# Kernel optimization log

Hardware: AMD Instinct MI355X
Metric: run time of the kernel (lower is better)

The kernel has to match this reference:

```python
import jax, jax.numpy as jnp
import numpy as np

H = 1.0  # RBF bandwidth (init kwarg h)


def setup_inputs() -> dict:
    key = jax.random.key(0)
    k1, k2 = jax.random.split(key)
    x = jax.random.normal(k1, (8192, 512), dtype=jnp.float32)
    x1 = jax.random.normal(k2, (8192, 512), dtype=jnp.float32)
    return {"x": x, "x1": x1}


def reference(x, x1):
    # exp(-||x_i - x1_j||^2 / h), computed via the GEMM trick to avoid the
    # O(N*M*D) broadcast intermediate the original torch code materializes.
    x_sq = jnp.sum(x * x, axis=-1, keepdims=True)          # [N, 1]
    x1_sq = jnp.sum(x1 * x1, axis=-1)                       # [M]
    cross = jnp.einsum('nd,md->nm', x, x1)                  # [N, M]
    d = jnp.maximum(x_sq + x1_sq[None, :] - 2.0 * cross, 0.0)
    return jnp.exp(-d / H)
```

## Files before the change

kernel.cpp:

```cpp
#include <hip/hip_runtime.h>
#include <stdint.h>
#include <stddef.h>


#define NROWS 8192
#define DIMK  512
#define BM    128
#define BN    128
#define BKB   128
#define KT    (DIMK / BKB)

typedef __bf16 bf16x8 __attribute__((ext_vector_type(8)));
typedef int    i32x8  __attribute__((ext_vector_type(8)));
typedef float  f32x4  __attribute__((ext_vector_type(4)));

#define AS1 __attribute__((address_space(1)))
#define AS3 __attribute__((address_space(3)))

__device__ __forceinline__ uint32_t f2bf(float f) {
    uint32_t u = __float_as_uint(f);
    return (u + 0x7FFFu + ((u >> 16) & 1u)) >> 16;
}

__device__ __forceinline__ uint32_t f2e4m3(float f) {
    uint32_t u   = __float_as_uint(f);
    uint32_t s   = (u >> 24) & 0x80u;
    uint32_t abs = u & 0x7FFFFFFFu;
    if (abs >= 0x43E00000u)
        return s | 0x7Eu;
    if (abs < 0x3C800000u) {
        uint32_t m = (uint32_t)rintf(__uint_as_float(abs) * 512.0f);
        return s | m;
    }
    uint32_t lsb = (abs >> 20) & 1u;
    uint32_t r   = abs + 0x7FFFFu + lsb;
    uint32_t e   = (r >> 23) - 127u + 7u;
    uint32_t m   = (r >> 20) & 7u;
    return s | (e << 3) | m;
}

__global__ __launch_bounds__(256) void precast_fp8(
    const float* __restrict__ x, const float* __restrict__ x1,
    uint8_t* __restrict__ xf, uint8_t* __restrict__ x1f,
    float* __restrict__ xsq, float* __restrict__ x1sq)
{
    const int w    = threadIdx.x >> 6;
    const int lane = threadIdx.x & 63;
    const int row  = blockIdx.x * 4 + w;
    const float* src;
    uint8_t* dstb;
    float* dsts;
    if (blockIdx.y == 0) { src = x  + (size_t)row * DIMK; dstb = xf  + (size_t)row * DIMK; dsts = xsq  + row; }
    else                 { src = x1 + (size_t)row * DIMK; dstb = x1f + (size_t)row * DIMK; dsts = x1sq + row; }

    float4 v0 = ((const float4*)src)[lane * 2];
    float4 v1 = ((const float4*)src)[lane * 2 + 1];
    float s = v0.x * v0.x + v0.y * v0.y + v0.z * v0.z + v0.w * v0.w
            + v1.x * v1.x + v1.y * v1.y + v1.z * v1.z + v1.w * v1.w;

    uint2 p;
    p.x = f2e4m3(v0.x) | (f2e4m3(v0.y) << 8) | (f2e4m3(v0.z) << 16) | (f2e4m3(v0.w) << 24);
    p.y = f2e4m3(v1.x) | (f2e4m3(v1.y) << 8) | (f2e4m3(v1.z) << 16) | (f2e4m3(v1.w) << 24);
    ((uint2*)dstb)[lane] = p;

    #pragma unroll
    for (int off = 32; off > 0; off >>= 1) s += __shfl_down(s, off);
    if (lane == 0) *dsts = s;
}

__global__ __launch_bounds__(256) void norms_only(
    const float* __restrict__ x, const float* __restrict__ x1,
    float* __restrict__ xsq, float* __restrict__ x1sq)
{
    const int row = blockIdx.x;
    const float* src = (blockIdx.y == 0) ? x + (size_t)row * DIMK : x1 + (size_t)row * DIMK;
    float* dsts      = (blockIdx.y == 0) ? xsq + row : x1sq + row;
    const int t = threadIdx.x;
    float2 v = ((const float2*)src)[t];
    float s = v.x * v.x + v.y * v.y;
    #pragma unroll
    for (int off = 32; off > 0; off >>= 1) s += __shfl_down(s, off);
    __shared__ float red[4];
    if ((t & 63) == 0) red[t >> 6] = s;
    __syncthreads();
    if (t == 0) *dsts = red[0] + red[1] + red[2] + red[3];
}

__global__ __launch_bounds__(256) void rbf_mfma_mxfp8(
    const uint8_t* __restrict__ Xf, const uint8_t* __restrict__ X1f,
    const float* __restrict__ xsq, const float* __restrict__ x1sq,
    float* __restrict__ out)
{
    __shared__ uint8_t As[BM * BKB];
    __shared__ uint8_t Bs[BN * BKB];

    const int t    = threadIdx.x;
    const int bm   = blockIdx.x;
    const int bn   = blockIdx.y;
    const int lane = t & 63;
    const int w    = t >> 6;
    const int wm   = w >> 1;
    const int wn   = w & 1;

    const int srow = t >> 3;
    const int scol = (t & 7) * 16;
    const uint8_t* gA = Xf  + (size_t)(bm * BM + srow) * DIMK + scol;
    const uint8_t* gB = X1f + (size_t)(bn * BN + srow) * DIMK + scol;
    uint8_t* lA = &As[t * 16];
    uint8_t* lB = &Bs[t * 16];

    const int lrow = lane & 15;
    const int row0 = bm * BM + wm * 64 + (lane >> 4) * 4;
    const int col0 = bn * BN + wn * 64 + lrow;
    float xs[4][4], x1s[4];
    #pragma unroll
    for (int tm = 0; tm < 4; ++tm)
        #pragma unroll
        for (int r = 0; r < 4; ++r) xs[tm][r] = xsq[row0 + tm * 16 + r];
    #pragma unroll
    for (int tn = 0; tn < 4; ++tn) x1s[tn] = x1sq[col0 + tn * 16];

    f32x4 acc[4][4];
    #pragma unroll
    for (int i = 0; i < 4; ++i)
        #pragma unroll
        for (int j = 0; j < 4; ++j)
            acc[i][j] = f32x4{0.f, 0.f, 0.f, 0.f};

    const int kq = (lane >> 4) * 32;
    int aoff[4], boff[4];
    #pragma unroll
    for (int i = 0; i < 4; ++i) {
        aoff[i] = (wm * 64 + i * 16 + lrow) * BKB + kq;
        boff[i] = (wn * 64 + i * 16 + lrow) * BKB + kq;
    }

    #pragma unroll
    for (int kt = 0; kt < KT; ++kt) {
        const uint8_t* ga = gA + kt * BKB;
        const uint8_t* gb = gB + kt * BKB;
        #pragma unroll
        for (int c = 0; c < 4; ++c) {
            __builtin_amdgcn_global_load_lds((AS1 void*)(ga + (size_t)c * 32 * DIMK),
                                             (AS3 void*)(lA + c * 4096), 16, 0, 0);
            __builtin_amdgcn_global_load_lds((AS1 void*)(gb + (size_t)c * 32 * DIMK),
                                             (AS3 void*)(lB + c * 4096), 16, 0, 0);
        }
        __syncthreads();

        i32x8 af[4], bg[4];
        #pragma unroll
        for (int i = 0; i < 4; ++i) af[i] = *(const i32x8*)&As[aoff[i]];
        #pragma unroll
        for (int i = 0; i < 4; ++i) bg[i] = *(const i32x8*)&Bs[boff[i]];
        #pragma unroll
        for (int i = 0; i < 4; ++i)
            #pragma unroll
            for (int j = 0; j < 4; ++j)
                acc[i][j] = __builtin_amdgcn_mfma_scale_f32_16x16x128_f8f6f4(
                    af[i], bg[j], acc[i][j],
                    0, 0,
                    0, 0x7F7F7F7F,
                    0, 0x7F7F7F7F);
        __syncthreads();
    }

    #pragma unroll
    for (int tm = 0; tm < 4; ++tm)
        #pragma unroll
        for (int tn = 0; tn < 4; ++tn)
            #pragma unroll
            for (int r = 0; r < 4; ++r) {
                const int row = row0 + tm * 16 + r;
                const int col = col0 + tn * 16;
                float d = xs[tm][r] + x1s[tn] - 2.0f * acc[tm][tn][r];
                d = fmaxf(d, 0.0f);
                out[(size_t)row * NROWS + col] = __expf(-d);
            }
}

__global__ __launch_bounds__(256) void rbf_mfma_inline(
    const float* __restrict__ X, const float* __restrict__ X1,
    const float* __restrict__ xsq, const float* __restrict__ x1sq,
    float* __restrict__ out)
{
    __shared__ uint16_t As[BM * 32];
    __shared__ uint16_t Bs[BN * 32];

    const int t    = threadIdx.x;
    const int bm   = blockIdx.x;
    const int bn   = blockIdx.y;
    const int lane = t & 63;
    const int w    = t >> 6;
    const int wm   = w >> 1;
    const int wn   = w & 1;

    f32x4 acc[4][4];
    #pragma unroll
    for (int i = 0; i < 4; ++i)
        #pragma unroll
        for (int j = 0; j < 4; ++j)
            acc[i][j] = f32x4{0.f, 0.f, 0.f, 0.f};

    const int lrow = lane & 15;
    const int kq   = (lane >> 4) * 8;
    int aoff[4], boff[4];
    #pragma unroll
    for (int i = 0; i < 4; ++i) {
        aoff[i] = (wm * 64 + i * 16 + lrow) * 32 + kq;
        boff[i] = (wn * 64 + i * 16 + lrow) * 32 + kq;
    }

    for (int kt = 0; kt < DIMK / 32; ++kt) {
        #pragma unroll
        for (int i = 0; i < 4; ++i) {
            const int g   = t + i * 256;
            const int row = g >> 3;
            const int c4  = (g & 7) * 4;
            float4 va = *(const float4*)&X [(size_t)(bm * BM + row) * DIMK + kt * 32 + c4];
            float4 vb = *(const float4*)&X1[(size_t)(bn * BN + row) * DIMK + kt * 32 + c4];
            uint2 pa, pb;
            pa.x = f2bf(va.x) | (f2bf(va.y) << 16);
            pa.y = f2bf(va.z) | (f2bf(va.w) << 16);
            pb.x = f2bf(vb.x) | (f2bf(vb.y) << 16);
            pb.y = f2bf(vb.z) | (f2bf(vb.w) << 16);
            *(uint2*)&As[g * 4] = pa;
            *(uint2*)&Bs[g * 4] = pb;
        }
        __syncthreads();

        bf16x8 af[4], bg[4];
        #pragma unroll
        for (int i = 0; i < 4; ++i) af[i] = *(const bf16x8*)&As[aoff[i]];
        #pragma unroll
        for (int i = 0; i < 4; ++i) bg[i] = *(const bf16x8*)&Bs[boff[i]];
        #pragma unroll
        for (int i = 0; i < 4; ++i)
            #pragma unroll
            for (int j = 0; j < 4; ++j)
                acc[i][j] = __builtin_amdgcn_mfma_f32_16x16x32_bf16(af[i], bg[j], acc[i][j], 0, 0, 0);
        __syncthreads();
    }

    const int row0 = bm * BM + wm * 64 + (lane >> 4) * 4;
    const int col0 = bn * BN + wn * 64 + lrow;
    float xs[4][4], x1s[4];
    #pragma unroll
    for (int tm = 0; tm < 4; ++tm)
        #pragma unroll
        for (int r = 0; r < 4; ++r) xs[tm][r] = xsq[row0 + tm * 16 + r];
    #pragma unroll
    for (int tn = 0; tn < 4; ++tn) x1s[tn] = x1sq[col0 + tn * 16];

    #pragma unroll
    for (int tm = 0; tm < 4; ++tm)
        #pragma unroll
        for (int tn = 0; tn < 4; ++tn)
            #pragma unroll
            for (int r = 0; r < 4; ++r) {
                const int row = row0 + tm * 16 + r;
                const int col = col0 + tn * 16;
                float d = xs[tm][r] + x1s[tn] - 2.0f * acc[tm][tn][r];
                d = fmaxf(d, 0.0f);
                out[(size_t)row * NROWS + col] = __expf(-d);
            }
}

extern "C" void kernel_launch(void* const* d_in, const int* in_sizes, int n_in,
                              void* d_out, int out_size, void* d_ws, size_t ws_size,
                              hipStream_t stream)
{
    const float* x  = (const float*)d_in[0];
    const float* x1 = (const float*)d_in[1];
    float* out = (float*)d_out;

    const size_t f8_bytes  = (size_t)NROWS * DIMK;
    const size_t need_full = 2 * f8_bytes + 2 * (size_t)NROWS * sizeof(float);

    dim3 gridG(NROWS / BM, NROWS / BN);

    if (ws_size >= need_full) {
        uint8_t* xf   = (uint8_t*)d_ws;
        uint8_t* x1f  = xf + f8_bytes;
        float*   xsq  = (float*)((char*)d_ws + 2 * f8_bytes);
        float*   x1sq = xsq + NROWS;
        precast_fp8<<<dim3(NROWS / 4, 2), 256, 0, stream>>>(x, x1, xf, x1f, xsq, x1sq);
        rbf_mfma_mxfp8<<<gridG, 256, 0, stream>>>(xf, x1f, xsq, x1sq, out);
    } else {
        float* xsq  = (float*)d_ws;
        float* x1sq = xsq + NROWS;
        norms_only<<<dim3(NROWS, 2), 256, 0, stream>>>(x, x1, xsq, x1sq);
        rbf_mfma_inline<<<gridG, 256, 0, stream>>>(x, x1, xsq, x1sq, out);
    }
}
```

Measured before the change: 314.2 us.

## Use hardware fp8 conversion, tune occupancy, defer norm loads, nontemporal output stores

```diff
diff --git a/kernel.cpp b/kernel.cpp
--- a/kernel.cpp
+++ b/kernel.cpp
@@ -22,21 +22,10 @@
     return (u + 0x7FFFu + ((u >> 16) & 1u)) >> 16;
 }
 
-__device__ __forceinline__ uint32_t f2e4m3(float f) {
-    uint32_t u   = __float_as_uint(f);
-    uint32_t s   = (u >> 24) & 0x80u;
-    uint32_t abs = u & 0x7FFFFFFFu;
-    if (abs >= 0x43E00000u)
-        return s | 0x7Eu;
-    if (abs < 0x3C800000u) {
-        uint32_t m = (uint32_t)rintf(__uint_as_float(abs) * 512.0f);
-        return s | m;
-    }
-    uint32_t lsb = (abs >> 20) & 1u;
-    uint32_t r   = abs + 0x7FFFFu + lsb;
-    uint32_t e   = (r >> 23) - 127u + 7u;
-    uint32_t m   = (r >> 20) & 7u;
-    return s | (e << 3) | m;
+__device__ __forceinline__ uint32_t pk_fp8x4(float a, float b, float c, float d) {
+    int w = __builtin_amdgcn_cvt_pk_fp8_f32(a, b, 0, false);
+    w     = __builtin_amdgcn_cvt_pk_fp8_f32(c, d, w, true);
+    return (uint32_t)w;
 }
 
 __global__ __launch_bounds__(256) void precast_fp8(
@@ -59,8 +48,8 @@
             + v1.x * v1.x + v1.y * v1.y + v1.z * v1.z + v1.w * v1.w;
 
     uint2 p;
-    p.x = f2e4m3(v0.x) | (f2e4m3(v0.y) << 8) | (f2e4m3(v0.z) << 16) | (f2e4m3(v0.w) << 24);
-    p.y = f2e4m3(v1.x) | (f2e4m3(v1.y) << 8) | (f2e4m3(v1.z) << 16) | (f2e4m3(v1.w) << 24);
+    p.x = pk_fp8x4(v0.x, v0.y, v0.z, v0.w);
+    p.y = pk_fp8x4(v1.x, v1.y, v1.z, v1.w);
     ((uint2*)dstb)[lane] = p;
 
     #pragma unroll
@@ -86,7 +75,7 @@
     if (t == 0) *dsts = red[0] + red[1] + red[2] + red[3];
 }
 
-__global__ __launch_bounds__(256) void rbf_mfma_mxfp8(
+__global__ __launch_bounds__(256, 3) void rbf_mfma_mxfp8(
     const uint8_t* __restrict__ Xf, const uint8_t* __restrict__ X1f,
     const float* __restrict__ xsq, const float* __restrict__ x1sq,
     float* __restrict__ out)
@@ -109,17 +98,6 @@
     uint8_t* lA = &As[t * 16];
     uint8_t* lB = &Bs[t * 16];
 
-    const int lrow = lane & 15;
-    const int row0 = bm * BM + wm * 64 + (lane >> 4) * 4;
-    const int col0 = bn * BN + wn * 64 + lrow;
-    float xs[4][4], x1s[4];
-    #pragma unroll
-    for (int tm = 0; tm < 4; ++tm)
-        #pragma unroll
-        for (int r = 0; r < 4; ++r) xs[tm][r] = xsq[row0 + tm * 16 + r];
-    #pragma unroll
-    for (int tn = 0; tn < 4; ++tn) x1s[tn] = x1sq[col0 + tn * 16];
-
     f32x4 acc[4][4];
     #pragma unroll
     for (int i = 0; i < 4; ++i)
@@ -127,7 +105,8 @@
         for (int j = 0; j < 4; ++j)
             acc[i][j] = f32x4{0.f, 0.f, 0.f, 0.f};
 
-    const int kq = (lane >> 4) * 32;
+    const int lrow = lane & 15;
+    const int kq   = (lane >> 4) * 32;
     int aoff[4], boff[4];
     #pragma unroll
     for (int i = 0; i < 4; ++i) {
@@ -135,7 +114,7 @@
         boff[i] = (wn * 64 + i * 16 + lrow) * BKB + kq;
     }
 
-    #pragma unroll
+    #pragma unroll 1
     for (int kt = 0; kt < KT; ++kt) {
         const uint8_t* ga = gA + kt * BKB;
         const uint8_t* gb = gB + kt * BKB;
@@ -162,8 +141,18 @@
                     0, 0,
                     0, 0x7F7F7F7F,
                     0, 0x7F7F7F7F);
-        __syncthreads();
-    }
+        if (kt + 1 < KT) __syncthreads();
+    }
+
+    const int row0 = bm * BM + wm * 64 + (lane >> 4) * 4;
+    const int col0 = bn * BN + wn * 64 + lrow;
+    float xs[4][4], x1s[4];
+    #pragma unroll
+    for (int tm = 0; tm < 4; ++tm)
+        #pragma unroll
+        for (int r = 0; r < 4; ++r) xs[tm][r] = xsq[row0 + tm * 16 + r];
+    #pragma unroll
+    for (int tn = 0; tn < 4; ++tn) x1s[tn] = x1sq[col0 + tn * 16];
 
     #pragma unroll
     for (int tm = 0; tm < 4; ++tm)
@@ -175,7 +164,7 @@
                 const int col = col0 + tn * 16;
                 float d = xs[tm][r] + x1s[tn] - 2.0f * acc[tm][tn][r];
                 d = fmaxf(d, 0.0f);
-                out[(size_t)row * NROWS + col] = __expf(-d);
+                __builtin_nontemporal_store(__expf(-d), &out[(size_t)row * NROWS + col]);
             }
 }
 
@@ -211,6 +200,7 @@
         boff[i] = (wn * 64 + i * 16 + lrow) * 32 + kq;
     }
 
+    #pragma unroll 1
     for (int kt = 0; kt < DIMK / 32; ++kt) {
         #pragma unroll
         for (int i = 0; i < 4; ++i) {
```

After: 319.2 us. No clear change (+1.6%).
